# Kernel optimization log

Measured on AMD Instinct MI355X. Metric: run time of the kernel, lower is better.

The kernel has to match this reference:

```python
import jax, jax.numpy as jnp
import numpy as np

LMAX, MMAX = 4, 2
C_SPH = 32           # sphere_channels
H = 128              # edge hidden channels
N_SPECIES = 90
RESCALE = 5.0
M_SIZE_0 = LMAX + 1                                   # 5
NUM_COEFFS = sum(2 * min(l, MMAX) + 1 for l in range(LMAX + 1))  # 19
K_FULL = (LMAX + 1) ** 2                              # 25
N_NODES = 20000
N_EDGES = 320000
D_EDGE = 128
EPS = 1e-6


def layer_norm(x, scale, bias):
    mu = jnp.mean(x, axis=-1, keepdims=True)
    var = jnp.mean(jnp.square(x - mu), axis=-1, keepdims=True)
    return (x - mu) * jax.lax.rsqrt(var + EPS) * scale + bias


def setup_inputs() -> dict:
    key = jax.random.key(0)
    ks = jax.random.split(key, 12)
    node_species = jax.random.randint(ks[0], (N_NODES,), 0, N_SPECIES)
    edge_embeds = jax.random.normal(ks[1], (N_EDGES, D_EDGE), dtype=jnp.float32)
    senders = jax.random.randint(ks[2], (N_EDGES,), 0, N_NODES)
    receivers = jax.random.randint(ks[3], (N_EDGES,), 0, N_NODES)
    wigner_inv = jax.random.normal(ks[4], (N_EDGES, K_FULL, NUM_COEFFS), dtype=jnp.float32)
    # learned params
    embed_table = jax.random.normal(ks[5], (N_SPECIES, 2 * H), dtype=jnp.float32) * 0.001
    d_in = D_EDGE + 2 * H  # concat(edge, sender_emb, receiver_emb)
    W0 = jax.random.normal(ks[6], (d_in, H), dtype=jnp.float32) / np.sqrt(d_in)
    b0 = jnp.zeros((H,), jnp.float32)
    ln0_s = jnp.ones((H,), jnp.float32); ln0_b = jnp.zeros((H,), jnp.float32)
    W1 = jax.random.normal(ks[7], (H, H), dtype=jnp.float32) / np.sqrt(H)
    b1 = jnp.zeros((H,), jnp.float32)
    ln1_s = jnp.ones((H,), jnp.float32); ln1_b = jnp.zeros((H,), jnp.float32)
    W2 = jax.random.normal(ks[8], (H, M_SIZE_0 * C_SPH), dtype=jnp.float32) / np.sqrt(H)
    b2 = jnp.zeros((M_SIZE_0 * C_SPH,), jnp.float32)
    return dict(node_species=node_species, edge_embeds=edge_embeds, senders=senders,
                receivers=receivers, wigner_inv=wigner_inv, embed_table=embed_table,
                W0=W0, b0=b0, ln0_s=ln0_s, ln0_b=ln0_b,
                W1=W1, b1=b1, ln1_s=ln1_s, ln1_b=ln1_b, W2=W2, b2=b2)


def reference(node_species, edge_embeds, senders, receivers, wigner_inv, embed_table,
              W0, b0, ln0_s, ln0_b, W1, b1, ln1_s, ln1_b, W2, b2):
    num_nodes = node_species.shape[0]
    # atom edge embedding: gather + split
    node_emb = embed_table[node_species]                       # [N, 2H]
    s_emb, r_emb = jnp.split(node_emb, 2, axis=-1)             # [N, H] each
    x = jnp.concatenate((edge_embeds, s_emb[senders], r_emb[receivers]), axis=-1)  # [E, D+2H]
    # MLP with layer norm + silu between layers
    x = jax.nn.silu(layer_norm(x @ W0 + b0, ln0_s, ln0_b))
    x = jax.nn.silu(layer_norm(x @ W1 + b1, ln1_s, ln1_b))
    x = x @ W2 + b2                                            # [E, m0*C]
    feats_m_0 = x.reshape(-1, M_SIZE_0, C_SPH)                 # [E, 5, C]
    pad = jnp.zeros((x.shape[0], NUM_COEFFS - M_SIZE_0, C_SPH), dtype=x.dtype)
    edge_feats = jnp.concatenate((feats_m_0, pad), axis=1)     # [E, 19, C]
    # inverse wigner rotation back to full SH basis: [E, 25, C]
    edge_feats = jnp.einsum('ekm,emc->ekc', wigner_inv, edge_feats)
    node_feats = jax.ops.segment_sum(edge_feats, receivers, num_segments=num_nodes)
    return node_feats / RESCALE
```

## Files before the change

### kernel.cpp

```cpp
#include <hip/hip_runtime.h>
#include <hip/hip_bf16.h>
#include <cstddef>


#define MB 64
#define MTHREADS 512
#define DIN 384
#define HDIM 128
#define NOUT 160
#define NKF 25
#define WIG_LD 19
#define WIG_ROW 475

#define WP1OFF 98304
#define WP2OFF 131072
#define WPBYTES 172032

#define XS_B   784
#define FS_B   528
#define HS_B   272
#define REG0   0
#define REG1   50176
#define METAS  67584
#define METAR  67840
#define LDSSZ  68096

typedef __attribute__((ext_vector_type(8))) short short8;
typedef __attribute__((ext_vector_type(4))) float f32x4;

struct BF4 { __hip_bfloat162 a, b; };

__device__ __forceinline__ unsigned short f2bf(float f)
{
    union { float f; unsigned u; } x; x.f = f;
    unsigned r = x.u + 0x7fffu + ((x.u >> 16) & 1u);
    return (unsigned short)(r >> 16);
}

__global__ void repack_w(const float* __restrict__ W0, const float* __restrict__ W1,
                         const float* __restrict__ W2, unsigned short* __restrict__ Wp)
{
    const int id = blockIdx.x * 256 + threadIdx.x;
    const float* W; int k, n, NT, N; size_t base;
    if (id < 49152)      { W = W0; k = id >> 7;  n = id & 127;  NT = 8;  N = 128; base = 0; }
    else if (id < 65536) { int r = id - 49152; W = W1; k = r >> 7; n = r & 127; NT = 8; N = 128; base = 49152; }
    else if (id < 86016) { int r = id - 65536; W = W2; k = r / 160; n = r - 160 * k; NT = 10; N = 160; base = 65536; }
    else return;
    const float w = W[(size_t)k * N + n];
    const int kt = k >> 5, kk = k & 31;
    const int l = ((kk >> 3) << 4) | (n & 15);
    const int i = kk & 7;
    const int nt = n >> 4;
    Wp[base + (size_t)(kt * NT + nt) * 512 + l * 8 + i] = f2bf(w);
}

template<int NT, int KT>
__device__ __forceinline__ void gemm_tiles4(const char* __restrict__ ldsA, int astride,
                                            const char* __restrict__ wp,
                                            int nt, int lane, f32x4 acc[4])
{
    const int lr = lane & 15, lk = lane >> 4;
    short8 bcur = *(const short8*)(wp + (size_t)nt * 1024 + lane * 16);
#pragma unroll
    for (int kt = 0; kt < KT; ++kt) {
        short8 bnxt = bcur;
        if (kt + 1 < KT)
            bnxt = *(const short8*)(wp + (size_t)((kt + 1) * NT + nt) * 1024 + lane * 16);
        short8 a[4];
#pragma unroll
        for (int mt = 0; mt < 4; ++mt)
            a[mt] = *(const short8*)(ldsA + (mt * 16 + lr) * astride + kt * 64 + lk * 16);
#pragma unroll
        for (int mt = 0; mt < 4; ++mt)
            acc[mt] = __builtin_amdgcn_mfma_f32_16x16x32_bf16(a[mt], bcur, acc[mt], 0, 0, 0);
        bcur = bnxt;
    }
}

__device__ __forceinline__ void dump_acc4(char* Hf, int nt, int lane, const f32x4 acc[4],
                                          const float bias)
{
    const int lr = lane & 15, lk = lane >> 4;
#pragma unroll
    for (int mt = 0; mt < 4; ++mt)
#pragma unroll
        for (int i = 0; i < 4; ++i)
            *(float*)(Hf + (mt * 16 + lk * 4 + i) * FS_B + (nt * 16 + lr) * 4) = acc[mt][i] + bias;
}

__device__ __forceinline__ void ln_silu_bf(const char* Hf, char* Hb,
                                           const float* __restrict__ s,
                                           const float* __restrict__ b, int t)
{
    const int j = t & 7;
    const int r = t >> 3;
    float v[16];
    float sum = 0.f, sq = 0.f;
#pragma unroll
    for (int q4 = 0; q4 < 4; ++q4) {
        const float4 x4 = *(const float4*)(Hf + r * FS_B + (j * 16 + q4 * 4) * 4);
        v[q4 * 4 + 0] = x4.x; v[q4 * 4 + 1] = x4.y;
        v[q4 * 4 + 2] = x4.z; v[q4 * 4 + 3] = x4.w;
    }
#pragma unroll
    for (int q = 0; q < 16; ++q) { sum += v[q]; sq = fmaf(v[q], v[q], sq); }
#pragma unroll
    for (int m = 1; m < 8; m <<= 1) {
        sum += __shfl_xor(sum, m, 64);
        sq  += __shfl_xor(sq,  m, 64);
    }
    const float mu = sum * (1.f / 128.f);
    const float var = sq * (1.f / 128.f) - mu * mu;
    const float rstd = rsqrtf(var + 1e-6f);
#pragma unroll
    for (int q = 0; q < 16; q += 2) {
        const int c0 = j * 16 + q;
        float y0 = (v[q] - mu) * rstd * s[c0] + b[c0];
        float y1 = (v[q + 1] - mu) * rstd * s[c0 + 1] + b[c0 + 1];
        y0 = y0 / (1.f + __expf(-y0));
        y1 = y1 / (1.f + __expf(-y1));
        *(__hip_bfloat162*)(Hb + r * HS_B + c0 * 2) =
            __float22bfloat162_rn(make_float2(y0, y1));
    }
}

__global__ __launch_bounds__(MTHREADS, 2)
void mlp_mfma(
    const int* __restrict__ species,
    const float* __restrict__ edge_embeds,
    const int* __restrict__ senders,
    const int* __restrict__ receivers,
    const float* __restrict__ embed_table,
    const char* __restrict__ Wp,
    const float* __restrict__ b0, const float* __restrict__ ln0s, const float* __restrict__ ln0b,
    const float* __restrict__ b1, const float* __restrict__ ln1s, const float* __restrict__ ln1b,
    const float* __restrict__ b2,
    float* __restrict__ F,
    int n_edges)
{
    __shared__ alignas(16) char lds[LDSSZ];
    int* sS = (int*)(lds + METAS);
    int* rS = (int*)(lds + METAR);

    const int t = threadIdx.x;
    const int e0 = blockIdx.x * MB;
    const int w = t >> 6;
    const int lane = t & 63;
    const int lr = lane & 15, lk = lane >> 4;

    if (t < MB) {
        const int e = e0 + t;
        int s = 0, r = 0;
        if (e < n_edges) { s = senders[e]; r = receivers[e]; }
        sS[t] = species[s];
        rS[t] = species[r];
    }
    __syncthreads();

    {
        const int row = t >> 3;
        const int e = e0 + row;
        const bool ev = e < n_edges;
        const int ss = sS[row], rr = rS[row];
        char* xrow = lds + REG0 + row * XS_B;
        const int c0 = (t & 7) * 4;
#pragma unroll
        for (int jj = 0; jj < 12; ++jj) {
            const int col = c0 + 32 * jj;
            float4 v = make_float4(0.f, 0.f, 0.f, 0.f);
            if (ev) {
                if (jj < 4)
                    v = *(const float4*)(edge_embeds + (size_t)e * 128 + col);
                else if (jj < 8)
                    v = *(const float4*)(embed_table + (size_t)ss * 256 + (col - 128));
                else
                    v = *(const float4*)(embed_table + (size_t)rr * 256 + 128 + (col - 256));
            }
            BF4 pk;
            pk.a = __float22bfloat162_rn(make_float2(v.x, v.y));
            pk.b = __float22bfloat162_rn(make_float2(v.z, v.w));
            *(BF4*)(xrow + col * 2) = pk;
        }
    }
    __syncthreads();

    const char* wp0 = Wp;
    const char* wp1 = Wp + WP1OFF;
    const char* wp2 = Wp + WP2OFF;

    f32x4 acc[4];

#pragma unroll
    for (int mt = 0; mt < 4; ++mt) acc[mt] = (f32x4){0.f, 0.f, 0.f, 0.f};
    gemm_tiles4<8, 12>(lds + REG0, XS_B, wp0, w, lane, acc);
    __syncthreads();
    dump_acc4(lds + REG0, w, lane, acc, b0[w * 16 + lr]);
    __syncthreads();
    ln_silu_bf(lds + REG0, lds + REG1, ln0s, ln0b, t);
    __syncthreads();

#pragma unroll
    for (int mt = 0; mt < 4; ++mt) acc[mt] = (f32x4){0.f, 0.f, 0.f, 0.f};
    gemm_tiles4<8, 4>(lds + REG1, HS_B, wp1, w, lane, acc);
    dump_acc4(lds + REG0, w, lane, acc, b1[w * 16 + lr]);
    __syncthreads();
    ln_silu_bf(lds + REG0, lds + REG1, ln1s, ln1b, t);
    __syncthreads();

#pragma unroll
    for (int p = 0; p < 2; ++p) {
        const int nt = w + 8 * p;
        if (nt >= 10) break;
#pragma unroll
        for (int mt = 0; mt < 4; ++mt) acc[mt] = (f32x4){0.f, 0.f, 0.f, 0.f};
        gemm_tiles4<10, 4>(lds + REG1, HS_B, wp2, nt, lane, acc);
        const float bb = b2[nt * 16 + lr];
#pragma unroll
        for (int mt = 0; mt < 4; ++mt)
#pragma unroll
            for (int i = 0; i < 4; ++i) {
                const int e = e0 + mt * 16 + lk * 4 + i;
                if (e < n_edges)
                    F[(size_t)e * NOUT + nt * 16 + lr] = (acc[mt][i] + bb) * 0.2f;
            }
    }
}

__global__ void hist_kernel(const int* __restrict__ recv, int* __restrict__ cnt, int n_edges)
{
    const int e = blockIdx.x * 256 + threadIdx.x;
    if (e < n_edges) atomicAdd(&cnt[recv[e]], 1);
}

#define SCAN_T 1024
#define SCAN_CH 20
__global__ __launch_bounds__(SCAN_T)
void scan_kernel(const int* __restrict__ cnt, int* __restrict__ offsets,
                 int* __restrict__ cursor, int n_nodes)
{
    __shared__ int waveSum[SCAN_T / 64];
    const int t = threadIdx.x;
    const int base = t * SCAN_CH;
    int local[SCAN_CH];
    int s = 0;
#pragma unroll
    for (int j = 0; j < SCAN_CH; ++j) {
        const int v = (base + j < n_nodes) ? cnt[base + j] : 0;
        local[j] = s;
        s += v;
    }
    const int lane = t & 63;
    int incl = s;
#pragma unroll
    for (int d = 1; d < 64; d <<= 1) {
        const int u = __shfl_up(incl, d, 64);
        if (lane >= d) incl += u;
    }
    if (lane == 63) waveSum[t >> 6] = incl;
    __syncthreads();
    if (t < SCAN_T / 64) {
        const int v = waveSum[t];
        int incl2 = v;
#pragma unroll
        for (int d = 1; d < SCAN_T / 64; d <<= 1) {
            const int u = __shfl_up(incl2, d, 64);
            if (lane >= d) incl2 += u;
        }
        waveSum[t] = incl2 - v;
    }
    __syncthreads();
    const int threadExcl = waveSum[t >> 6] + (incl - s);
#pragma unroll
    for (int j = 0; j < SCAN_CH; ++j)
        if (base + j < n_nodes) {
            const int o = threadExcl + local[j];
            offsets[base + j] = o;
            cursor[base + j] = o;
        }
    if (t == SCAN_T - 1) offsets[n_nodes] = threadExcl + s;
}

__global__ void scatter_kernel(const int* __restrict__ recv, int* __restrict__ cursor,
                               int* __restrict__ elist, int n_edges)
{
    const int e = blockIdx.x * 256 + threadIdx.x;
    if (e < n_edges) {
        const int p = atomicAdd(&cursor[recv[e]], 1);
        elist[p] = e;
    }
}

__global__ __launch_bounds__(256)
void agg_kernel(const float* __restrict__ wigner, const float* __restrict__ F,
                const int* __restrict__ offsets, const int* __restrict__ elist,
                float* __restrict__ out)
{
    const int n = blockIdx.x;
    const int t = threadIdx.x;
    __shared__ float wigS[2][128];

    const int beg = offsets[n];
    const int end = offsets[n + 1];

    const int ch = t & 31;
    const int k0 = t >> 5;
    float a0 = 0.f, a1 = 0.f, a2 = 0.f, a3 = 0.f;

    float f[5];
    if (beg < end) {
        const int e = elist[beg];
        if (t < 125) wigS[0][t] = wigner[(size_t)e * WIG_ROW + (t / 5) * WIG_LD + (t % 5)];
        const float* Fp = F + (size_t)e * NOUT + ch;
#pragma unroll
        for (int m = 0; m < 5; ++m) f[m] = Fp[m * 32];
    }

    int buf = 0;
    for (int i = beg; i < end; ++i) {
        __syncthreads();
        float fc[5];
#pragma unroll
        for (int m = 0; m < 5; ++m) fc[m] = f[m];
        if (i + 1 < end) {
            const int e = elist[i + 1];
            if (t < 125) wigS[buf ^ 1][t] = wigner[(size_t)e * WIG_ROW + (t / 5) * WIG_LD + (t % 5)];
            const float* Fp = F + (size_t)e * NOUT + ch;
#pragma unroll
            for (int m = 0; m < 5; ++m) f[m] = Fp[m * 32];
        }
        const float* wp = &wigS[buf][0];
        { const float* wq = wp + k0 * 5;        a0 += wq[0]*fc[0] + wq[1]*fc[1] + wq[2]*fc[2] + wq[3]*fc[3] + wq[4]*fc[4]; }
        { const float* wq = wp + (k0 + 8) * 5;  a1 += wq[0]*fc[0] + wq[1]*fc[1] + wq[2]*fc[2] + wq[3]*fc[3] + wq[4]*fc[4]; }
        { const float* wq = wp + (k0 + 16) * 5; a2 += wq[0]*fc[0] + wq[1]*fc[1] + wq[2]*fc[2] + wq[3]*fc[3] + wq[4]*fc[4]; }
        if (t < 32) { const float* wq = wp + 120; a3 += wq[0]*fc[0] + wq[1]*fc[1] + wq[2]*fc[2] + wq[3]*fc[3] + wq[4]*fc[4]; }
        buf ^= 1;
    }

    float* orow = out + (size_t)n * (NKF * 32);
    orow[t] = a0;
    orow[t + 256] = a1;
    orow[t + 512] = a2;
    if (t < 32) orow[t + 768] = a3;
}

#define EB 32
__device__ __forceinline__ void ln_silu_f(float (*Bx)[HDIM], const float* __restrict__ s,
                                          const float* __restrict__ b, int t)
{
    const int r = t >> 3;
    const int j = t & 7;
    float v[16];
    float sum = 0.f, sq = 0.f;
#pragma unroll
    for (int q = 0; q < 16; ++q) { v[q] = Bx[r][j*16+q]; sum += v[q]; sq = fmaf(v[q], v[q], sq); }
#pragma unroll
    for (int m = 1; m < 8; m <<= 1) { sum += __shfl_xor(sum, m, 64); sq += __shfl_xor(sq, m, 64); }
    const float mu = sum * (1.f/HDIM);
    const float var = sq * (1.f/HDIM) - mu*mu;
    const float rstd = rsqrtf(var + 1e-6f);
#pragma unroll
    for (int q = 0; q < 16; ++q) {
        const int cc = j*16+q;
        const float y = (v[q]-mu)*rstd*s[cc]+b[cc];
        Bx[r][cc] = y / (1.f + __expf(-y));
    }
}

__global__ __launch_bounds__(256, 2)
void edge_fused_kernel(
    const int* __restrict__ species, const float* __restrict__ edge_embeds,
    const int* __restrict__ senders, const int* __restrict__ receivers,
    const float* __restrict__ wigner, const float* __restrict__ embed_table,
    const float* __restrict__ W0, const float* __restrict__ b0,
    const float* __restrict__ ln0s, const float* __restrict__ ln0b,
    const float* __restrict__ W1, const float* __restrict__ b1,
    const float* __restrict__ ln1s, const float* __restrict__ ln1b,
    const float* __restrict__ W2, const float* __restrict__ b2,
    float* __restrict__ out, int n_edges)
{
    __shared__ float A[EB][DIN];
    __shared__ float Bx[EB][HDIM];
    __shared__ int sSpec[EB], rSpec[EB], rNode[EB];
    const int t = threadIdx.x;
    const int e0 = blockIdx.x * EB;
    if (t < EB) {
        const int e = e0 + t;
        int s = 0, r = 0;
        if (e < n_edges) { s = senders[e]; r = receivers[e]; }
        sSpec[t] = species[s]; rSpec[t] = species[r]; rNode[t] = r;
    }
    __syncthreads();
    for (int idx = t; idx < EB * DIN; idx += 256) {
        const int r = idx / DIN;
        const int i = idx - r * DIN;
        const int e = e0 + r;
        float v = 0.f;
        if (e < n_edges) {
            if (i < HDIM) v = edge_embeds[(size_t)e * HDIM + i];
            else if (i < 2*HDIM) v = embed_table[(size_t)sSpec[r]*256 + (i-HDIM)];
            else v = embed_table[(size_t)rSpec[r]*256 + HDIM + (i-2*HDIM)];
        }
        A[r][i] = v;
    }
    __syncthreads();
    const int c = t & (HDIM-1);
    const int g = t >> 7;
    float acc[16];
#pragma unroll
    for (int q = 0; q < 16; ++q) acc[q] = 0.f;
    for (int it = 0; it < DIN/4; ++it) {
        const float wa = W0[(4*it+0)*HDIM+c], wb = W0[(4*it+1)*HDIM+c];
        const float wc = W0[(4*it+2)*HDIM+c], wd = W0[(4*it+3)*HDIM+c];
#pragma unroll
        for (int q = 0; q < 16; ++q) {
            const float4 x4 = *reinterpret_cast<const float4*>(&A[g*16+q][4*it]);
            acc[q] = fmaf(x4.x, wa, fmaf(x4.y, wb, fmaf(x4.z, wc, fmaf(x4.w, wd, acc[q]))));
        }
    }
    { const float bb = b0[c];
#pragma unroll
      for (int q = 0; q < 16; ++q) Bx[g*16+q][c] = acc[q] + bb; }
    __syncthreads(); ln_silu_f(Bx, ln0s, ln0b, t); __syncthreads();
#pragma unroll
    for (int q = 0; q < 16; ++q) acc[q] = 0.f;
    for (int it = 0; it < HDIM/4; ++it) {
        const float wa = W1[(4*it+0)*HDIM+c], wb = W1[(4*it+1)*HDIM+c];
        const float wc = W1[(4*it+2)*HDIM+c], wd = W1[(4*it+3)*HDIM+c];
#pragma unroll
        for (int q = 0; q < 16; ++q) {
            const float4 x4 = *reinterpret_cast<const float4*>(&Bx[g*16+q][4*it]);
            acc[q] = fmaf(x4.x, wa, fmaf(x4.y, wb, fmaf(x4.z, wc, fmaf(x4.w, wd, acc[q]))));
        }
    }
    __syncthreads();
    { const float bb = b1[c];
#pragma unroll
      for (int q = 0; q < 16; ++q) Bx[g*16+q][c] = acc[q] + bb; }
    __syncthreads(); ln_silu_f(Bx, ln1s, ln1b, t); __syncthreads();
    float* Ff = &A[0][0];
    {
        float a2[16];
#pragma unroll
        for (int q = 0; q < 16; ++q) a2[q] = 0.f;
        for (int it = 0; it < HDIM/4; ++it) {
            const float wa = W2[(4*it+0)*NOUT+c], wb = W2[(4*it+1)*NOUT+c];
            const float wc = W2[(4*it+2)*NOUT+c], wd = W2[(4*it+3)*NOUT+c];
#pragma unroll
            for (int q = 0; q < 16; ++q) {
                const float4 x4 = *reinterpret_cast<const float4*>(&Bx[g*16+q][4*it]);
                a2[q] = fmaf(x4.x, wa, fmaf(x4.y, wb, fmaf(x4.z, wc, fmaf(x4.w, wd, a2[q]))));
            }
        }
        const float bb = b2[c];
#pragma unroll
        for (int q = 0; q < 16; ++q) Ff[(g*16+q)*NOUT+c] = (a2[q]+bb)*0.2f;
    }
    {
        const int c2 = HDIM + (t & 31);
        const int g8 = t >> 5;
        float a2[4] = {0.f, 0.f, 0.f, 0.f};
        for (int it = 0; it < HDIM/4; ++it) {
            const float wa = W2[(4*it+0)*NOUT+c2], wb = W2[(4*it+1)*NOUT+c2];
            const float wc = W2[(4*it+2)*NOUT+c2], wd = W2[(4*it+3)*NOUT+c2];
#pragma unroll
            for (int q = 0; q < 4; ++q) {
                const float4 x4 = *reinterpret_cast<const float4*>(&Bx[g8*4+q][4*it]);
                a2[q] = fmaf(x4.x, wa, fmaf(x4.y, wb, fmaf(x4.z, wc, fmaf(x4.w, wd, a2[q]))));
            }
        }
        const float bb = b2[c2];
#pragma unroll
        for (int q = 0; q < 4; ++q) Ff[(g8*4+q)*NOUT+c2] = (a2[q]+bb)*0.2f;
    }
    __syncthreads();
    for (int r = 0; r < EB; ++r) {
        const int e = e0 + r;
        if (e >= n_edges) break;
        const float* wrow = wigner + (size_t)e * WIG_ROW;
        float* orow = out + (size_t)rNode[r] * (NKF*32);
        const float* Fr = Ff + r * NOUT;
#pragma unroll
        for (int jj = 0; jj < 4; ++jj) {
            const int p = t + 256*jj;
            if (p < NKF*32) {
                const int k = p >> 5, chh = p & 31;
                float val = 0.f;
#pragma unroll
                for (int m = 0; m < 5; ++m)
                    val = fmaf(wrow[k*WIG_LD+m], Fr[m*32+chh], val);
                atomicAdd(&orow[p], val);
            }
        }
    }
}

extern "C" void kernel_launch(void* const* d_in, const int* in_sizes, int n_in,
                              void* d_out, int out_size, void* d_ws, size_t ws_size,
                              hipStream_t stream)
{
    const int*   species     = (const int*)d_in[0];
    const float* edge_embeds = (const float*)d_in[1];
    const int*   senders     = (const int*)d_in[2];
    const int*   receivers   = (const int*)d_in[3];
    const float* wigner      = (const float*)d_in[4];
    const float* embed_table = (const float*)d_in[5];
    const float* W0 = (const float*)d_in[6];
    const float* b0 = (const float*)d_in[7];
    const float* ln0s = (const float*)d_in[8];
    const float* ln0b = (const float*)d_in[9];
    const float* W1 = (const float*)d_in[10];
    const float* b1 = (const float*)d_in[11];
    const float* ln1s = (const float*)d_in[12];
    const float* ln1b = (const float*)d_in[13];
    const float* W2 = (const float*)d_in[14];
    const float* b2 = (const float*)d_in[15];
    float* out = (float*)d_out;

    const int n_nodes = in_sizes[0];
    const int n_edges = in_sizes[2];

    const size_t wpBytes   = WPBYTES;
    const size_t fBytes    = (size_t)n_edges * NOUT * sizeof(float);
    const size_t offBytes  = (size_t)(n_nodes + 1) * sizeof(int);
    const size_t curBytes  = (size_t)n_nodes * sizeof(int);
    const size_t listBytes = (size_t)n_edges * sizeof(int);
    const size_t need = wpBytes + fBytes + offBytes + curBytes + listBytes + 64;

    if (ws_size < need || n_nodes > SCAN_T * SCAN_CH || n_edges <= 0) {
        hipMemsetAsync(out, 0, (size_t)out_size * sizeof(float), stream);
        const int nblocks = (n_edges + EB - 1) / EB;
        hipLaunchKernelGGL(edge_fused_kernel, dim3(nblocks), dim3(256), 0, stream,
                           species, edge_embeds, senders, receivers, wigner, embed_table,
                           W0, b0, ln0s, ln0b, W1, b1, ln1s, ln1b, W2, b2, out, n_edges);
        return;
    }

    char* ws = (char*)d_ws;
    unsigned short* Wp = (unsigned short*)ws;
    float* F       = (float*)(ws + wpBytes);
    int*   offsets = (int*)(ws + wpBytes + fBytes);
    int*   cursor  = (int*)(ws + wpBytes + fBytes + offBytes);
    int*   elist   = (int*)(ws + wpBytes + fBytes + offBytes + curBytes);

    const int egrid = (n_edges + 255) / 256;

    hipLaunchKernelGGL(repack_w, dim3(336), dim3(256), 0, stream, W0, W1, W2, Wp);

    hipMemsetAsync(cursor, 0, curBytes, stream);
    hipLaunchKernelGGL(hist_kernel, dim3(egrid), dim3(256), 0, stream,
                       receivers, cursor, n_edges);
    hipLaunchKernelGGL(scan_kernel, dim3(1), dim3(SCAN_T), 0, stream,
                       cursor, offsets, cursor, n_nodes);
    hipLaunchKernelGGL(scatter_kernel, dim3(egrid), dim3(256), 0, stream,
                       receivers, cursor, elist, n_edges);

    const int mblocks = (n_edges + MB - 1) / MB;
    hipLaunchKernelGGL(mlp_mfma, dim3(mblocks), dim3(MTHREADS), 0, stream,
                       species, edge_embeds, senders, receivers, embed_table,
                       (const char*)Wp, b0, ln0s, ln0b, b1, ln1s, ln1b, b2, F, n_edges);

    hipLaunchKernelGGL(agg_kernel, dim3(n_nodes), dim3(256), 0, stream,
                       wigner, F, offsets, elist, out);
}
```

Measured before the change: 502.3 us.

## Store edge MLP output in bf16 and fold histogram/scatter into neighbouring kernels

The intermediate per-edge feature buffer F is now written as bf16 instead of fp32, which halves the bytes the MLP writes and the aggregation kernel reads. The histogram is merged into the weight-repack launch, and the CSR scatter into extra blocks of the MLP launch, which removes two kernel launches. In exchange, the intermediate loses precision before the wigner contraction and segment sum. The scatter blocks now share a launch with the MLP blocks, and the MLP blocks get their offset from sgrid.

```diff
diff --git a/kernel.cpp b/kernel.cpp
--- a/kernel.cpp
+++ b/kernel.cpp
@@ -37,10 +37,18 @@
     return (unsigned short)(r >> 16);
 }
 
-__global__ void repack_w(const float* __restrict__ W0, const float* __restrict__ W1,
-                         const float* __restrict__ W2, unsigned short* __restrict__ Wp)
-{
-    const int id = blockIdx.x * 256 + threadIdx.x;
+__global__ void pre_kernel(const int* __restrict__ recv, int* __restrict__ cnt,
+                           int n_edges, int hgrid,
+                           const float* __restrict__ W0, const float* __restrict__ W1,
+                           const float* __restrict__ W2, unsigned short* __restrict__ Wp)
+{
+    const int bid = blockIdx.x;
+    if (bid < hgrid) {
+        const int e = bid * 256 + threadIdx.x;
+        if (e < n_edges) atomicAdd(&cnt[recv[e]], 1);
+        return;
+    }
+    const int id = (bid - hgrid) * 256 + threadIdx.x;
     const float* W; int k, n, NT, N; size_t base;
     if (id < 49152)      { W = W0; k = id >> 7;  n = id & 127;  NT = 8;  N = 128; base = 0; }
     else if (id < 65536) { int r = id - 49152; W = W1; k = r >> 7; n = r & 127; NT = 8; N = 128; base = 49152; }
@@ -135,15 +143,28 @@
     const float* __restrict__ b0, const float* __restrict__ ln0s, const float* __restrict__ ln0b,
     const float* __restrict__ b1, const float* __restrict__ ln1s, const float* __restrict__ ln1b,
     const float* __restrict__ b2,
-    float* __restrict__ F,
+    __hip_bfloat16* __restrict__ F,
+    int* __restrict__ cursor, int* __restrict__ elist, int sgrid,
     int n_edges)
 {
     __shared__ alignas(16) char lds[LDSSZ];
+
+    const int bid = blockIdx.x;
+    const int t = threadIdx.x;
+
+    if (bid < sgrid) {
+        const int e = bid * MTHREADS + t;
+        if (e < n_edges) {
+            const int p = atomicAdd(&cursor[receivers[e]], 1);
+            elist[p] = e;
+        }
+        return;
+    }
+
     int* sS = (int*)(lds + METAS);
     int* rS = (int*)(lds + METAR);
 
-    const int t = threadIdx.x;
-    const int e0 = blockIdx.x * MB;
+    const int e0 = (bid - sgrid) * MB;
     const int w = t >> 6;
     const int lane = t & 63;
     const int lr = lane & 15, lk = lane >> 4;
@@ -220,16 +241,13 @@
 #pragma unroll
             for (int i = 0; i < 4; ++i) {
                 const int e = e0 + mt * 16 + lk * 4 + i;
-                if (e < n_edges)
-                    F[(size_t)e * NOUT + nt * 16 + lr] = (acc[mt][i] + bb) * 0.2f;
+                if (e < n_edges) {
+                    union { unsigned short u; __hip_bfloat16 h; } cv;
+                    cv.u = f2bf((acc[mt][i] + bb) * 0.2f);
+                    F[(size_t)e * NOUT + nt * 16 + lr] = cv.h;
+                }
             }
     }
-}
-
-__global__ void hist_kernel(const int* __restrict__ recv, int* __restrict__ cnt, int n_edges)
-{
-    const int e = blockIdx.x * 256 + threadIdx.x;
-    if (e < n_edges) atomicAdd(&cnt[recv[e]], 1);
 }
 
 #define SCAN_T 1024
@@ -280,18 +298,8 @@
     if (t == SCAN_T - 1) offsets[n_nodes] = threadExcl + s;
 }
 
-__global__ void scatter_kernel(const int* __restrict__ recv, int* __restrict__ cursor,
-                               int* __restrict__ elist, int n_edges)
-{
-    const int e = blockIdx.x * 256 + threadIdx.x;
-    if (e < n_edges) {
-        const int p = atomicAdd(&cursor[recv[e]], 1);
-        elist[p] = e;
-    }
-}
-
 __global__ __launch_bounds__(256)
-void agg_kernel(const float* __restrict__ wigner, const float* __restrict__ F,
+void agg_kernel(const float* __restrict__ wigner, const __hip_bfloat16* __restrict__ F,
                 const int* __restrict__ offsets, const int* __restrict__ elist,
                 float* __restrict__ out)
 {
@@ -310,9 +318,9 @@
     if (beg < end) {
         const int e = elist[beg];
         if (t < 125) wigS[0][t] = wigner[(size_t)e * WIG_ROW + (t / 5) * WIG_LD + (t % 5)];
-        const float* Fp = F + (size_t)e * NOUT + ch;
-#pragma unroll
-        for (int m = 0; m < 5; ++m) f[m] = Fp[m * 32];
+        const __hip_bfloat16* Fp = F + (size_t)e * NOUT + ch;
+#pragma unroll
+        for (int m = 0; m < 5; ++m) f[m] = __bfloat162float(Fp[m * 32]);
     }
 
     int buf = 0;
@@ -324,9 +332,9 @@
         if (i + 1 < end) {
             const int e = elist[i + 1];
             if (t < 125) wigS[buf ^ 1][t] = wigner[(size_t)e * WIG_ROW + (t / 5) * WIG_LD + (t % 5)];
-            const float* Fp = F + (size_t)e * NOUT + ch;
-#pragma unroll
-            for (int m = 0; m < 5; ++m) f[m] = Fp[m * 32];
+            const __hip_bfloat16* Fp = F + (size_t)e * NOUT + ch;
+#pragma unroll
+            for (int m = 0; m < 5; ++m) f[m] = __bfloat162float(Fp[m * 32]);
         }
         const float* wp = &wigS[buf][0];
         { const float* wq = wp + k0 * 5;        a0 += wq[0]*fc[0] + wq[1]*fc[1] + wq[2]*fc[2] + wq[3]*fc[3] + wq[4]*fc[4]; }
@@ -520,7 +528,7 @@
     const int n_edges = in_sizes[2];
 
     const size_t wpBytes   = WPBYTES;
-    const size_t fBytes    = (size_t)n_edges * NOUT * sizeof(float);
+    const size_t fBytes    = (size_t)n_edges * NOUT * sizeof(unsigned short);
     const size_t offBytes  = (size_t)(n_nodes + 1) * sizeof(int);
     const size_t curBytes  = (size_t)n_nodes * sizeof(int);
     const size_t listBytes = (size_t)n_edges * sizeof(int);
@@ -537,27 +545,26 @@
 
     char* ws = (char*)d_ws;
     unsigned short* Wp = (unsigned short*)ws;
-    float* F       = (float*)(ws + wpBytes);
+    __hip_bfloat16* F  = (__hip_bfloat16*)(ws + wpBytes);
     int*   offsets = (int*)(ws + wpBytes + fBytes);
     int*   cursor  = (int*)(ws + wpBytes + fBytes + offBytes);
     int*   elist   = (int*)(ws + wpBytes + fBytes + offBytes + curBytes);
 
-    const int egrid = (n_edges + 255) / 256;
-
-    hipLaunchKernelGGL(repack_w, dim3(336), dim3(256), 0, stream, W0, W1, W2, Wp);
+    const int hgrid = (n_edges + 255) / 256;
 
     hipMemsetAsync(cursor, 0, curBytes, stream);
-    hipLaunchKernelGGL(hist_kernel, dim3(egrid), dim3(256), 0, stream,
-                       receivers, cursor, n_edges);
+    hipLaunchKernelGGL(pre_kernel, dim3(hgrid + 336), dim3(256), 0, stream,
+                       receivers, cursor, n_edges, hgrid, W0, W1, W2, Wp);
+
     hipLaunchKernelGGL(scan_kernel, dim3(1), dim3(SCAN_T), 0, stream,
                        cursor, offsets, cursor, n_nodes);
-    hipLaunchKernelGGL(scatter_kernel, dim3(egrid), dim3(256), 0, stream,
-                       receivers, cursor, elist, n_edges);
-
+
+    const int sgrid = (n_edges + MTHREADS - 1) / MTHREADS;
     const int mblocks = (n_edges + MB - 1) / MB;
-    hipLaunchKernelGGL(mlp_mfma, dim3(mblocks), dim3(MTHREADS), 0, stream,
+    hipLaunchKernelGGL(mlp_mfma, dim3(sgrid + mblocks), dim3(MTHREADS), 0, stream,
                        species, edge_embeds, senders, receivers, embed_table,
-                       (const char*)Wp, b0, ln0s, ln0b, b1, ln1s, ln1b, b2, F, n_edges);
+                       (const char*)Wp, b0, ln0s, ln0b, b1, ln1s, ln1b, b2,
+                       F, cursor, elist, sgrid, n_edges);
 
     hipLaunchKernelGGL(agg_kernel, dim3(n_nodes), dim3(256), 0, stream,
                        wigner, F, offsets, elist, out);
```

Result: faster. 479.5 us (median of 2 runs) (-4.5%).
